# Performance work log

Measured on AMD Instinct MI355X. Metric: run time of the kernel, lower is better.

The kernel has to match this reference:

```python
import jax, jax.numpy as jnp
import numpy as np

N_NODES = 30000


def gcn_conv(x, src, dst, ew, W, b, n):
    # x: [N, Fin] -> linear first (PyG GCNConv), then normalized scatter-add
    h = x @ W  # [N, Fout]
    loops = jnp.arange(n, dtype=src.dtype)
    s = jnp.concatenate([src, loops])
    d = jnp.concatenate([dst, loops])
    w = jnp.concatenate([ew, jnp.ones((n,), dtype=ew.dtype)])
    deg = jax.ops.segment_sum(w, d, num_segments=n)
    dinv = jnp.where(deg > 0, jax.lax.rsqrt(jnp.where(deg > 0, deg, 1.0)), 0.0)
    norm = dinv[s] * w * dinv[d]  # [E+N]
    msg = h[s] * norm[:, None]  # [E+N, Fout]
    out = jax.ops.segment_sum(msg, d, num_segments=n)
    return out + b


def setup_inputs() -> dict:
    key = jax.random.key(0)
    ks = jax.random.split(key, 16)
    n, e, f, c = N_NODES, 480000, 64, 64
    dims = [f, 2 * c, 4 * c, 8 * c]  # 64 -> 128 -> 256 -> 512
    num_classes = 40

    def lin(k, fi, fo):
        k1, k2 = jax.random.split(k)
        s = 1.0 / np.sqrt(fi)
        return (jax.random.uniform(k1, (fi, fo), jnp.float32, -s, s),
                jax.random.uniform(k2, (fo,), jnp.float32, -s, s))

    W1, b1 = lin(ks[0], dims[0], dims[1])
    W2, b2 = lin(ks[1], dims[1], dims[2])
    W3, b3 = lin(ks[2], dims[2], dims[3])
    fW1, fb1 = lin(ks[3], dims[3], dims[3])
    fW2, fb2 = lin(ks[4], dims[3], num_classes)
    return {
        "x": jax.random.normal(ks[5], (n, f), jnp.float32),
        "edge_index": jax.random.randint(ks[6], (2, e), 0, n, jnp.int32),
        "edge_attr": jax.random.uniform(ks[7], (e, 1), jnp.float32),
        "W1": W1, "b1": b1, "W2": W2, "b2": b2, "W3": W3, "b3": b3,
        "fW1": fW1, "fb1": fb1, "fW2": fW2, "fb2": fb2,
    }


def reference(x, edge_index, edge_attr, W1, b1, W2, b2, W3, b3, fW1, fb1, fW2, fb2):
    n = x.shape[0]
    src, dst = edge_index[0], edge_index[1]
    ew = edge_attr.squeeze(-1)
    h = jax.nn.relu(gcn_conv(x, src, dst, ew, W1, b1, n))
    h = jax.nn.relu(gcn_conv(h, src, dst, ew, W2, b2, n))
    h = jax.nn.relu(gcn_conv(h, src, dst, ew, W3, b3, n))
    h = jax.nn.relu(h @ fW1 + fb1)
    h = h @ fW2 + fb2
    return jax.nn.log_softmax(h, axis=1)
```

## Files before the change

### kernel.cpp

```cpp
#include <hip/hip_runtime.h>
#include <cstdint>
#include <cstddef>


typedef _Float16 f16;
typedef _Float16 half8 __attribute__((ext_vector_type(8)));
typedef _Float16 half4 __attribute__((ext_vector_type(4)));
typedef float v4f __attribute__((ext_vector_type(4)));
typedef unsigned long long u64;

__device__ inline void gload_lds16(const void* g, void* l) {
    __builtin_amdgcn_global_load_lds(
        (const __attribute__((address_space(1))) unsigned int*)g,
        (__attribute__((address_space(3))) unsigned int*)l, 16, 0, 0);
}


__global__ __launch_bounds__(256) void k_edge1(const int* __restrict__ dst, const float* __restrict__ ew,
                                               u64* __restrict__ packed4, int* __restrict__ eslot,
                                               int E, int n) {
    int t = blockIdx.x * blockDim.x + threadIdx.x;
    int e0 = t * 4;
    int r = t & 3;
    u64* plane = packed4 + (size_t)r * n;
    if (e0 + 3 < E) {
        int4 d4 = *(const int4*)(dst + e0);
        float4 w4 = *(const float4*)(ew + e0);
        u64 a0 = ((u64)__float2uint_rn(w4.x * 1048576.f) << 24) | 1ULL;
        u64 a1 = ((u64)__float2uint_rn(w4.y * 1048576.f) << 24) | 1ULL;
        u64 a2 = ((u64)__float2uint_rn(w4.z * 1048576.f) << 24) | 1ULL;
        u64 a3 = ((u64)__float2uint_rn(w4.w * 1048576.f) << 24) | 1ULL;
        u64 o0 = atomicAdd(&plane[d4.x], a0);
        u64 o1 = atomicAdd(&plane[d4.y], a1);
        u64 o2 = atomicAdd(&plane[d4.z], a2);
        u64 o3 = atomicAdd(&plane[d4.w], a3);
        int4 s;
        s.x = (int)(o0 & 0xFFFFFF); s.y = (int)(o1 & 0xFFFFFF);
        s.z = (int)(o2 & 0xFFFFFF); s.w = (int)(o3 & 0xFFFFFF);
        *(int4*)(eslot + e0) = s;
    } else {
        for (int e = e0; e < E; ++e) {
            u64 a = ((u64)__float2uint_rn(ew[e] * 1048576.f) << 24) | 1ULL;
            u64 o = atomicAdd(&plane[dst[e]], a);
            eslot[e] = (int)(o & 0xFFFFFF);
        }
    }
}

__global__ __launch_bounds__(256) void k_dinv_scan1(const u64* __restrict__ packed4,
                                                    float* __restrict__ dinv, int* __restrict__ cnt,
                                                    int4* __restrict__ rbase, int* __restrict__ bsum, int n) {
    int i = blockIdx.x * 256 + threadIdx.x;
    int c = 0;
    if (i < n) {
        u64 p0 = packed4[i];
        u64 p1 = packed4[(size_t)n + i];
        u64 p2 = packed4[(size_t)2 * n + i];
        u64 p3 = packed4[(size_t)3 * n + i];
        int c0 = (int)(p0 & 0xFFFFFF), c1 = (int)(p1 & 0xFFFFFF);
        int c2 = (int)(p2 & 0xFFFFFF), c3 = (int)(p3 & 0xFFFFFF);
        c = c0 + c1 + c2 + c3;
        rbase[i] = make_int4(0, c0, c0 + c1, c0 + c1 + c2);
        float d = 1.0f + (float)((p0 >> 24) + (p1 >> 24) + (p2 >> 24) + (p3 >> 24)) * (1.0f / 1048576.f);
        float r = rsqrtf(d);
        r = r * (1.5f - 0.5f * d * r * r);
        dinv[i] = r;
        cnt[i] = c;
    }
    int v = c;
#pragma unroll
    for (int o = 32; o; o >>= 1) v += __shfl_xor(v, o);
    __shared__ int s[4];
    if ((threadIdx.x & 63) == 0) s[threadIdx.x >> 6] = v;
    __syncthreads();
    if (threadIdx.x == 0) bsum[blockIdx.x] = s[0] + s[1] + s[2] + s[3];
}

__device__ inline int block_scan_incl(int v) {
    __shared__ int ws[4];
    int lane = threadIdx.x & 63, w = threadIdx.x >> 6;
#pragma unroll
    for (int off = 1; off < 64; off <<= 1) {
        int t = __shfl_up(v, off);
        if (lane >= off) v += t;
    }
    if (lane == 63) ws[w] = v;
    __syncthreads();
    int add = 0;
#pragma unroll
    for (int i = 0; i < 4; ++i) add += (i < w) ? ws[i] : 0;
    __syncthreads();
    return v + add;
}

__global__ __launch_bounds__(256) void k_scan23(const int* __restrict__ cnt, const int* __restrict__ bsum,
                                                int* __restrict__ rowptr, int n, int E) {
    int blk = blockIdx.x, tid = threadIdx.x;
    int i = blk * 256 + tid;
    __shared__ int spre;
    if (tid < 64) {
        int s = 0;
        for (int j = tid; j < blk; j += 64) s += bsum[j];
#pragma unroll
        for (int o = 32; o; o >>= 1) s += __shfl_xor(s, o);
        if (tid == 0) spre = s;
    }
    __syncthreads();
    int v = (i < n) ? cnt[i] : 0;
    int incl = block_scan_incl(v);
    if (i < n) rowptr[i] = spre + incl - v;
    if (i == n - 1) rowptr[n] = E;
}

__global__ __launch_bounds__(256) void k_fill(const int* __restrict__ src, const int* __restrict__ dst,
                                              const float* __restrict__ ew, const int* __restrict__ eslot,
                                              const float* __restrict__ dinv, const int* __restrict__ rowptr,
                                              const int4* __restrict__ rbase,
                                              int* __restrict__ csr_src, f16* __restrict__ csr_norm, int E) {
    int e = blockIdx.x * blockDim.x + threadIdx.x;
    if (e < E) {
        int d = dst[e], s = src[e];
        int r = (e >> 2) & 3;
        int4 rb = rbase[d];
        int base = (r == 0) ? rb.x : (r == 1) ? rb.y : (r == 2) ? rb.z : rb.w;
        int idx = rowptr[d] + base + eslot[e];
        csr_src[idx] = s;
        csr_norm[idx] = (f16)(dinv[s] * ew[e] * dinv[d]);
    }
}

struct PrepArgs {
    u64* packed4; int n4;
    const float* x; f16* xh; int xt4;
    const float* W[5]; f16* WT[5];
    int lgK[5]; int lgNp[5]; int N[5]; int off[6];
};
__global__ __launch_bounds__(256) void k_prep(PrepArgs a) {
    int i = blockIdx.x * 256 + threadIdx.x;
    if (i < a.n4) { a.packed4[i] = 0ULL; return; }
    int j = i - a.n4;
    if (j < a.xt4) {
        float4 v = *(const float4*)(a.x + (size_t)j * 4);
        half4 h = {(f16)v.x, (f16)v.y, (f16)v.z, (f16)v.w};
        *(half4*)(a.xh + (size_t)j * 4) = h;
        return;
    }
    int w = j - a.xt4;
#pragma unroll
    for (int s = 0; s < 5; ++s) {
        if (w >= a.off[s] && w < a.off[s + 1]) {
            int li = w - a.off[s];
            int Np = 1 << a.lgNp[s];
            int K = 1 << a.lgK[s];
            int k = li >> a.lgNp[s], nr = li & (Np - 1);
            float v = (nr < a.N[s]) ? a.W[s][(size_t)k * a.N[s] + nr] : 0.f;
            a.WT[s][(size_t)nr * K + k] = (f16)v;
        }
    }
}

template <int F>
__global__ __launch_bounds__(256) void k_agg(const f16* __restrict__ h,
                                             const float* __restrict__ dinv, const int* __restrict__ rowptr,
                                             const int* __restrict__ csr_src, const f16* __restrict__ csr_norm,
                                             f16* __restrict__ o, int n) {
    constexpr int LPN = F / 8;
    constexpr int NPW = 64 / LPN;
    int wave = (int)((blockIdx.x * (unsigned)blockDim.x + threadIdx.x) >> 6);
    int lane = threadIdx.x & 63;
    int grp = lane / LPN, lin = lane % LPN;
    int node = wave * NPW + grp;
    if (node >= n) return;
    float di = dinv[node], w0 = di * di;
    float acc[8];
#pragma unroll
    for (int i = 0; i < 8; ++i) acc[i] = 0.f;

    auto gat = [&](int s, float w) {
        half8 x = *(const half8*)(h + (size_t)s * F + lin * 8);
#pragma unroll
        for (int i = 0; i < 8; ++i) acc[i] += w * (float)x[i];
    };

    gat(node, w0);
    int beg = rowptr[node], end = rowptr[node + 1];
    int j = beg;
    for (; j + 3 < end; j += 4) {
        int s0 = csr_src[j], s1 = csr_src[j + 1], s2 = csr_src[j + 2], s3 = csr_src[j + 3];
        float u0 = (float)csr_norm[j], u1 = (float)csr_norm[j + 1];
        float u2 = (float)csr_norm[j + 2], u3 = (float)csr_norm[j + 3];
        gat(s0, u0); gat(s1, u1); gat(s2, u2); gat(s3, u3);
    }
    for (; j < end; ++j) gat(csr_src[j], (float)csr_norm[j]);

    half8 v;
#pragma unroll
    for (int i = 0; i < 8; ++i) v[i] = (f16)acc[i];
    *(half8*)(o + (size_t)node * F + (size_t)lin * 8) = v;
}

template <bool RELU>
__global__ __launch_bounds__(256) void k_mm(const f16* __restrict__ A, const f16* __restrict__ BT,
                                            const float* __restrict__ bias, f16* __restrict__ Ch,
                                            int M, int N, int K, int nB, int nwg) {
    __shared__ f16 lsA[2][128 * 64];
    __shared__ f16 lsB[2][128 * 64];
    int wg = blockIdx.x;
    int q = nwg >> 3, r = nwg & 7;
    int xcd = wg & 7, lin = wg >> 3;
    int wgs = (xcd < r) ? (xcd * (q + 1) + lin) : (r * (q + 1) + (xcd - r) * q + lin);
    int bm = wgs / nB, bn = wgs % nB;

    int tid = threadIdx.x;
    int lane = tid & 63, wid = tid >> 6;
    int l16 = lane & 15, lhi = lane >> 4;
    int wm = (wid >> 1) * 64, wn = (wid & 1) * 64;
    int brow = bm * 128, bcol = bn * 128;

    v4f acc[4][4] = {};

    auto stageA = [&](int buf, int k0) {
#pragma unroll
        for (int it = 0; it < 4; ++it) {
            int b = it * 4096 + tid * 16;
            int row = b >> 7;
            int s = ((b >> 4) & 7) ^ (row & 7);
            gload_lds16(A + (size_t)(brow + row) * K + k0 + s * 8, ((char*)&lsA[buf][0]) + b);
        }
    };
    auto stageB = [&](int buf, int k0) {
#pragma unroll
        for (int it = 0; it < 4; ++it) {
            int b = it * 4096 + tid * 16;
            int row = b >> 7;
            int s = ((b >> 4) & 7) ^ (row & 7);
            gload_lds16(BT + (size_t)(bcol + row) * K + k0 + s * 8, ((char*)&lsB[buf][0]) + b);
        }
    };

    int nk = K >> 6;
    stageA(0, 0);
    stageB(0, 0);
    for (int kt = 0; kt < nk; ++kt) {
        int cur = kt & 1;
        __syncthreads();
        if (kt + 1 < nk) { stageA(cur ^ 1, (kt + 1) << 6); stageB(cur ^ 1, (kt + 1) << 6); }
#pragma unroll
        for (int ks = 0; ks < 2; ++ks) {
            half8 bf[4];
#pragma unroll
            for (int fn = 0; fn < 4; ++fn) {
                int row = wn + fn * 16 + l16;
                int sidx = (ks * 4 + lhi) ^ (row & 7);
                bf[fn] = *(const half8*)(&lsB[cur][0] + row * 64 + sidx * 8);
            }
#pragma unroll
            for (int fm = 0; fm < 4; ++fm) {
                int row = wm + fm * 16 + l16;
                int sidx = (ks * 4 + lhi) ^ (row & 7);
                half8 af = *(const half8*)(&lsA[cur][0] + row * 64 + sidx * 8);
#pragma unroll
                for (int fn = 0; fn < 4; ++fn)
                    acc[fm][fn] = __builtin_amdgcn_mfma_f32_16x16x32_f16(bf[fn], af, acc[fm][fn], 0, 0, 0);
            }
        }
    }
#pragma unroll
    for (int fm = 0; fm < 4; ++fm) {
        int m = brow + wm + fm * 16 + l16;
        if (m >= M) continue;
#pragma unroll
        for (int fn = 0; fn < 4; ++fn) {
            int nb = bcol + wn + fn * 16 + lhi * 4;
            v4f bv = *(const v4f*)(bias + nb);
            v4f v = acc[fm][fn] + bv;
            if (RELU) {
#pragma unroll
                for (int rr = 0; rr < 4; ++rr) v[rr] = fmaxf(v[rr], 0.f);
            }
            half4 hv = {(f16)v[0], (f16)v[1], (f16)v[2], (f16)v[3]};
            *(half4*)(Ch + (size_t)m * N + nb) = hv;
        }
    }
}

__global__ __launch_bounds__(256) void k_mmfc2(const f16* __restrict__ A, const f16* __restrict__ BT,
                                               const float* __restrict__ bias, float* __restrict__ out,
                                               int M, int K) {
    __shared__ f16 lsA[2][256 * 64];
    __shared__ f16 lsB[2][64 * 64];
    int bm = blockIdx.x;
    int tid = threadIdx.x;
    int lane = tid & 63, wid = tid >> 6;
    int l16 = lane & 15, lhi = lane >> 4;
    int wm = wid * 64;
    int brow = bm * 256;

    v4f acc[4][4] = {};

    auto stageA = [&](int buf, int k0) {
#pragma unroll
        for (int it = 0; it < 8; ++it) {
            int b = it * 4096 + tid * 16;
            int row = b >> 7;
            int s = ((b >> 4) & 7) ^ (row & 7);
            gload_lds16(A + (size_t)(brow + row) * K + k0 + s * 8, ((char*)&lsA[buf][0]) + b);
        }
    };
    auto stageB = [&](int buf, int k0) {
#pragma unroll
        for (int it = 0; it < 2; ++it) {
            int b = it * 4096 + tid * 16;
            int row = b >> 7;
            int s = ((b >> 4) & 7) ^ (row & 7);
            gload_lds16(BT + (size_t)row * K + k0 + s * 8, ((char*)&lsB[buf][0]) + b);
        }
    };

    int nk = K >> 6;
    stageA(0, 0);
    stageB(0, 0);
    for (int kt = 0; kt < nk; ++kt) {
        int cur = kt & 1;
        __syncthreads();
        if (kt + 1 < nk) { stageA(cur ^ 1, (kt + 1) << 6); stageB(cur ^ 1, (kt + 1) << 6); }
#pragma unroll
        for (int ks = 0; ks < 2; ++ks) {
            half8 bf[4];
#pragma unroll
            for (int fn = 0; fn < 4; ++fn) {
                int row = fn * 16 + l16;
                int sidx = (ks * 4 + lhi) ^ (row & 7);
                bf[fn] = *(const half8*)(&lsB[cur][0] + row * 64 + sidx * 8);
            }
#pragma unroll
            for (int fm = 0; fm < 4; ++fm) {
                int row = wm + fm * 16 + l16;
                int sidx = (ks * 4 + lhi) ^ (row & 7);
                half8 af = *(const half8*)(&lsA[cur][0] + row * 64 + sidx * 8);
#pragma unroll
                for (int fn = 0; fn < 4; ++fn)
                    acc[fm][fn] = __builtin_amdgcn_mfma_f32_16x16x32_f16(bf[fn], af, acc[fm][fn], 0, 0, 0);
            }
        }
    }

    float bv[4][4];
#pragma unroll
    for (int fn = 0; fn < 4; ++fn)
#pragma unroll
        for (int rr = 0; rr < 4; ++rr) {
            int nn = fn * 16 + lhi * 4 + rr;
            bv[fn][rr] = (nn < 40) ? bias[nn] : 0.f;
        }

#pragma unroll
    for (int fm = 0; fm < 4; ++fm) {
        int m = brow + wm + fm * 16 + l16;
        float v[4][4];
        float mx = -INFINITY;
#pragma unroll
        for (int fn = 0; fn < 4; ++fn)
#pragma unroll
            for (int rr = 0; rr < 4; ++rr) {
                int nn = fn * 16 + lhi * 4 + rr;
                v[fn][rr] = acc[fm][fn][rr] + bv[fn][rr];
                if (nn < 40) mx = fmaxf(mx, v[fn][rr]);
            }
        mx = fmaxf(mx, __shfl_xor(mx, 16));
        mx = fmaxf(mx, __shfl_xor(mx, 32));
        float s = 0.f;
#pragma unroll
        for (int fn = 0; fn < 3; ++fn)
#pragma unroll
            for (int rr = 0; rr < 4; ++rr) {
                int nn = fn * 16 + lhi * 4 + rr;
                if (nn < 40) s += __expf(v[fn][rr] - mx);
            }
        s += __shfl_xor(s, 16);
        s += __shfl_xor(s, 32);
        float ls = __logf(s);
        if (m < M) {
#pragma unroll
            for (int fn = 0; fn < 3; ++fn)
#pragma unroll
                for (int rr = 0; rr < 4; ++rr) {
                    int nn = fn * 16 + lhi * 4 + rr;
                    if (nn < 40) out[(size_t)m * 40 + nn] = v[fn][rr] - mx - ls;
                }
        }
    }
}


extern "C" void kernel_launch(void* const* d_in, const int* in_sizes, int n_in,
                              void* d_out, int out_size, void* d_ws, size_t ws_size,
                              hipStream_t stream) {
    const float* x   = (const float*)d_in[0];
    const int*   ei  = (const int*)d_in[1];
    const float* ea  = (const float*)d_in[2];
    const float* W1  = (const float*)d_in[3];  const float* b1  = (const float*)d_in[4];
    const float* W2  = (const float*)d_in[5];  const float* b2  = (const float*)d_in[6];
    const float* W3  = (const float*)d_in[7];  const float* b3  = (const float*)d_in[8];
    const float* fW1 = (const float*)d_in[9];  const float* fb1 = (const float*)d_in[10];
    const float* fW2 = (const float*)d_in[11]; const float* fb2 = (const float*)d_in[12];

    int n = in_sizes[0] / 64;
    int E = in_sizes[1] / 2;
    int Mpad = ((n + 255) / 256) * 256;
    const int* src = ei;
    const int* dst = ei + E;
    float* out = (float*)d_out;

    char* p = (char*)d_ws;
    auto alloc = [&](size_t bytes) -> char* {
        char* r = p;
        p += (bytes + 255) & ~(size_t)255;
        return r;
    };
    int nb256 = (n + 255) / 256;
    u64*   packed4  = (u64*)alloc((size_t)n * 4 * 8);
    float* dinv     = (float*)alloc((size_t)n * 4);
    int*   cnt      = (int*)alloc((size_t)n * 4);
    int4*  rbase    = (int4*)alloc((size_t)n * 16);
    int*   rowptr   = (int*)alloc((size_t)(n + 1) * 4);
    int*   bsum     = (int*)alloc((size_t)nb256 * 4);
    int*   eslot    = (int*)alloc((size_t)E * 4);
    int*   csr_src  = (int*)alloc((size_t)E * 4);
    f16*   csr_norm = (f16*)alloc((size_t)E * 2);
    f16* XH  = (f16*)alloc((size_t)Mpad * 64 * 2);
    f16* W1T = (f16*)alloc((size_t)128 * 64 * 2);
    f16* W2T = (f16*)alloc((size_t)256 * 128 * 2);
    f16* W3T = (f16*)alloc((size_t)512 * 256 * 2);
    f16* F1T = (f16*)alloc((size_t)512 * 512 * 2);
    f16* F2T = (f16*)alloc((size_t)64 * 512 * 2);
    f16* AGG = (f16*)alloc((size_t)Mpad * 256 * 2);
    f16* HA  = (f16*)alloc((size_t)Mpad * 512 * 2);
    f16* HB  = (f16*)alloc((size_t)Mpad * 512 * 2);

    const int tb = 256;
    int eB = (E + tb - 1) / tb;
    int e4B = (E / 4 + tb - 1) / tb + 1;
    auto aggB = [&](int npw) {
        long waves = (n + npw - 1) / npw;
        return (int)((waves * 64 + tb - 1) / tb);
    };

    {
        PrepArgs a;
        a.packed4 = packed4; a.n4 = n * 4;
        a.x = x; a.xh = XH; a.xt4 = n * 16;
        a.W[0] = W1;  a.WT[0] = W1T; a.lgK[0] = 6; a.lgNp[0] = 7; a.N[0] = 128;
        a.W[1] = W2;  a.WT[1] = W2T; a.lgK[1] = 7; a.lgNp[1] = 8; a.N[1] = 256;
        a.W[2] = W3;  a.WT[2] = W3T; a.lgK[2] = 8; a.lgNp[2] = 9; a.N[2] = 512;
        a.W[3] = fW1; a.WT[3] = F1T; a.lgK[3] = 9; a.lgNp[3] = 9; a.N[3] = 512;
        a.W[4] = fW2; a.WT[4] = F2T; a.lgK[4] = 9; a.lgNp[4] = 6; a.N[4] = 40;
        a.off[0] = 0;
        a.off[1] = a.off[0] + 128 * 64;
        a.off[2] = a.off[1] + 256 * 128;
        a.off[3] = a.off[2] + 512 * 256;
        a.off[4] = a.off[3] + 512 * 512;
        a.off[5] = a.off[4] + 64 * 512;
        int tot = a.n4 + a.xt4 + a.off[5];
        k_prep<<<(tot + tb - 1) / tb, tb, 0, stream>>>(a);
    }

    k_edge1<<<e4B, tb, 0, stream>>>(dst, ea, packed4, eslot, E, n);
    k_dinv_scan1<<<nb256, tb, 0, stream>>>(packed4, dinv, cnt, rbase, bsum, n);
    k_scan23<<<nb256, tb, 0, stream>>>(cnt, bsum, rowptr, n, E);
    k_fill<<<eB, tb, 0, stream>>>(src, dst, ea, eslot, dinv, rowptr, rbase, csr_src, csr_norm, E);

    auto mm = [&](const f16* a, const f16* bt, const float* bias, f16* ch, int N, int K) {
        int nB2 = N / 128;
        int nwg = (Mpad / 128) * nB2;
        k_mm<true><<<nwg, 256, 0, stream>>>(a, bt, bias, ch, n, N, K, nB2, nwg);
    };

    k_agg<64><<<aggB(8), tb, 0, stream>>>(XH, dinv, rowptr, csr_src, csr_norm, AGG, n);
    mm(AGG, W1T, b1, HA, 128, 64);
    k_agg<128><<<aggB(4), tb, 0, stream>>>(HA, dinv, rowptr, csr_src, csr_norm, AGG, n);
    mm(AGG, W2T, b2, HB, 256, 128);
    k_agg<256><<<aggB(2), tb, 0, stream>>>(HB, dinv, rowptr, csr_src, csr_norm, AGG, n);
    mm(AGG, W3T, b3, HA, 512, 256);
    mm(HA, F1T, fb1, HB, 512, 512);
    k_mmfc2<<<Mpad / 256, 256, 0, stream>>>(HB, F2T, fb2, out, n, 512);
}
```

Measured before the change: 199.1 us.

## Use single atomic counter plane and split aggregation accumulators

Replaces the four striped per-node atomic count/degree planes with one plane. This removes the rbase prefix array and its extra loads and stores in the scan and fill kernels, at the cost of more atomic contention per address. The aggregation kernel also unrolls the edge loop by 8 and alternates between two accumulator sets, giving more gathers in flight and shorter FP dependency chains, at the cost of more registers.

New measurement: 204.0 us. +2.5%, slower.

```diff
diff --git a/kernel.cpp b/kernel.cpp
--- a/kernel.cpp
+++ b/kernel.cpp
@@ -17,12 +17,9 @@
 
 
 __global__ __launch_bounds__(256) void k_edge1(const int* __restrict__ dst, const float* __restrict__ ew,
-                                               u64* __restrict__ packed4, int* __restrict__ eslot,
-                                               int E, int n) {
+                                               u64* __restrict__ packed, int* __restrict__ eslot, int E) {
     int t = blockIdx.x * blockDim.x + threadIdx.x;
     int e0 = t * 4;
-    int r = t & 3;
-    u64* plane = packed4 + (size_t)r * n;
     if (e0 + 3 < E) {
         int4 d4 = *(const int4*)(dst + e0);
         float4 w4 = *(const float4*)(ew + e0);
@@ -30,10 +27,10 @@
         u64 a1 = ((u64)__float2uint_rn(w4.y * 1048576.f) << 24) | 1ULL;
         u64 a2 = ((u64)__float2uint_rn(w4.z * 1048576.f) << 24) | 1ULL;
         u64 a3 = ((u64)__float2uint_rn(w4.w * 1048576.f) << 24) | 1ULL;
-        u64 o0 = atomicAdd(&plane[d4.x], a0);
-        u64 o1 = atomicAdd(&plane[d4.y], a1);
-        u64 o2 = atomicAdd(&plane[d4.z], a2);
-        u64 o3 = atomicAdd(&plane[d4.w], a3);
+        u64 o0 = atomicAdd(&packed[d4.x], a0);
+        u64 o1 = atomicAdd(&packed[d4.y], a1);
+        u64 o2 = atomicAdd(&packed[d4.z], a2);
+        u64 o3 = atomicAdd(&packed[d4.w], a3);
         int4 s;
         s.x = (int)(o0 & 0xFFFFFF); s.y = (int)(o1 & 0xFFFFFF);
         s.z = (int)(o2 & 0xFFFFFF); s.w = (int)(o3 & 0xFFFFFF);
@@ -41,27 +38,21 @@
     } else {
         for (int e = e0; e < E; ++e) {
             u64 a = ((u64)__float2uint_rn(ew[e] * 1048576.f) << 24) | 1ULL;
-            u64 o = atomicAdd(&plane[dst[e]], a);
+            u64 o = atomicAdd(&packed[dst[e]], a);
             eslot[e] = (int)(o & 0xFFFFFF);
         }
     }
 }
 
-__global__ __launch_bounds__(256) void k_dinv_scan1(const u64* __restrict__ packed4,
+__global__ __launch_bounds__(256) void k_dinv_scan1(const u64* __restrict__ packed,
                                                     float* __restrict__ dinv, int* __restrict__ cnt,
-                                                    int4* __restrict__ rbase, int* __restrict__ bsum, int n) {
+                                                    int* __restrict__ bsum, int n) {
     int i = blockIdx.x * 256 + threadIdx.x;
     int c = 0;
     if (i < n) {
-        u64 p0 = packed4[i];
-        u64 p1 = packed4[(size_t)n + i];
-        u64 p2 = packed4[(size_t)2 * n + i];
-        u64 p3 = packed4[(size_t)3 * n + i];
-        int c0 = (int)(p0 & 0xFFFFFF), c1 = (int)(p1 & 0xFFFFFF);
-        int c2 = (int)(p2 & 0xFFFFFF), c3 = (int)(p3 & 0xFFFFFF);
-        c = c0 + c1 + c2 + c3;
-        rbase[i] = make_int4(0, c0, c0 + c1, c0 + c1 + c2);
-        float d = 1.0f + (float)((p0 >> 24) + (p1 >> 24) + (p2 >> 24) + (p3 >> 24)) * (1.0f / 1048576.f);
+        u64 pk = packed[i];
+        c = (int)(pk & 0xFFFFFF);
+        float d = 1.0f + (float)(pk >> 24) * (1.0f / 1048576.f);
         float r = rsqrtf(d);
         r = r * (1.5f - 0.5f * d * r * r);
         dinv[i] = r;
@@ -115,30 +106,26 @@
 __global__ __launch_bounds__(256) void k_fill(const int* __restrict__ src, const int* __restrict__ dst,
                                               const float* __restrict__ ew, const int* __restrict__ eslot,
                                               const float* __restrict__ dinv, const int* __restrict__ rowptr,
-                                              const int4* __restrict__ rbase,
                                               int* __restrict__ csr_src, f16* __restrict__ csr_norm, int E) {
     int e = blockIdx.x * blockDim.x + threadIdx.x;
     if (e < E) {
         int d = dst[e], s = src[e];
-        int r = (e >> 2) & 3;
-        int4 rb = rbase[d];
-        int base = (r == 0) ? rb.x : (r == 1) ? rb.y : (r == 2) ? rb.z : rb.w;
-        int idx = rowptr[d] + base + eslot[e];
+        int idx = rowptr[d] + eslot[e];
         csr_src[idx] = s;
         csr_norm[idx] = (f16)(dinv[s] * ew[e] * dinv[d]);
     }
 }
 
 struct PrepArgs {
-    u64* packed4; int n4;
+    u64* packed; int n;
     const float* x; f16* xh; int xt4;
     const float* W[5]; f16* WT[5];
     int lgK[5]; int lgNp[5]; int N[5]; int off[6];
 };
 __global__ __launch_bounds__(256) void k_prep(PrepArgs a) {
     int i = blockIdx.x * 256 + threadIdx.x;
-    if (i < a.n4) { a.packed4[i] = 0ULL; return; }
-    int j = i - a.n4;
+    if (i < a.n) { a.packed[i] = 0ULL; return; }
+    int j = i - a.n;
     if (j < a.xt4) {
         float4 v = *(const float4*)(a.x + (size_t)j * 4);
         half4 h = {(f16)v.x, (f16)v.y, (f16)v.z, (f16)v.w};
@@ -172,30 +159,39 @@
     int node = wave * NPW + grp;
     if (node >= n) return;
     float di = dinv[node], w0 = di * di;
-    float acc[8];
-#pragma unroll
-    for (int i = 0; i < 8; ++i) acc[i] = 0.f;
-
-    auto gat = [&](int s, float w) {
+    float acca[8], accb[8];
+#pragma unroll
+    for (int i = 0; i < 8; ++i) { acca[i] = 0.f; accb[i] = 0.f; }
+
+    auto gat = [&](float* acc, int s, float w) {
         half8 x = *(const half8*)(h + (size_t)s * F + lin * 8);
 #pragma unroll
         for (int i = 0; i < 8; ++i) acc[i] += w * (float)x[i];
     };
 
-    gat(node, w0);
+    gat(acca, node, w0);
     int beg = rowptr[node], end = rowptr[node + 1];
     int j = beg;
-    for (; j + 3 < end; j += 4) {
+    for (; j + 7 < end; j += 8) {
         int s0 = csr_src[j], s1 = csr_src[j + 1], s2 = csr_src[j + 2], s3 = csr_src[j + 3];
+        int s4 = csr_src[j + 4], s5 = csr_src[j + 5], s6 = csr_src[j + 6], s7 = csr_src[j + 7];
         float u0 = (float)csr_norm[j], u1 = (float)csr_norm[j + 1];
         float u2 = (float)csr_norm[j + 2], u3 = (float)csr_norm[j + 3];
-        gat(s0, u0); gat(s1, u1); gat(s2, u2); gat(s3, u3);
-    }
-    for (; j < end; ++j) gat(csr_src[j], (float)csr_norm[j]);
+        float u4 = (float)csr_norm[j + 4], u5 = (float)csr_norm[j + 5];
+        float u6 = (float)csr_norm[j + 6], u7 = (float)csr_norm[j + 7];
+        gat(acca, s0, u0); gat(accb, s1, u1); gat(acca, s2, u2); gat(accb, s3, u3);
+        gat(acca, s4, u4); gat(accb, s5, u5); gat(acca, s6, u6); gat(accb, s7, u7);
+    }
+    for (; j + 1 < end; j += 2) {
+        int s0 = csr_src[j], s1 = csr_src[j + 1];
+        float u0 = (float)csr_norm[j], u1 = (float)csr_norm[j + 1];
+        gat(acca, s0, u0); gat(accb, s1, u1);
+    }
+    if (j < end) gat(acca, csr_src[j], (float)csr_norm[j]);
 
     half8 v;
 #pragma unroll
-    for (int i = 0; i < 8; ++i) v[i] = (f16)acc[i];
+    for (int i = 0; i < 8; ++i) v[i] = (f16)(acca[i] + accb[i]);
     *(half8*)(o + (size_t)node * F + (size_t)lin * 8) = v;
 }
 
@@ -419,10 +415,9 @@
         return r;
     };
     int nb256 = (n + 255) / 256;
-    u64*   packed4  = (u64*)alloc((size_t)n * 4 * 8);
+    u64*   packed   = (u64*)alloc((size_t)n * 8);
     float* dinv     = (float*)alloc((size_t)n * 4);
     int*   cnt      = (int*)alloc((size_t)n * 4);
-    int4*  rbase    = (int4*)alloc((size_t)n * 16);
     int*   rowptr   = (int*)alloc((size_t)(n + 1) * 4);
     int*   bsum     = (int*)alloc((size_t)nb256 * 4);
     int*   eslot    = (int*)alloc((size_t)E * 4);
@@ -448,7 +443,7 @@
 
     {
         PrepArgs a;
-        a.packed4 = packed4; a.n4 = n * 4;
+        a.packed = packed; a.n = n;
         a.x = x; a.xh = XH; a.xt4 = n * 16;
         a.W[0] = W1;  a.WT[0] = W1T; a.lgK[0] = 6; a.lgNp[0] = 7; a.N[0] = 128;
         a.W[1] = W2;  a.WT[1] = W2T; a.lgK[1] = 7; a.lgNp[1] = 8; a.N[1] = 256;
@@ -461,14 +456,14 @@
         a.off[3] = a.off[2] + 512 * 256;
         a.off[4] = a.off[3] + 512 * 512;
         a.off[5] = a.off[4] + 64 * 512;
-        int tot = a.n4 + a.xt4 + a.off[5];
+        int tot = a.n + a.xt4 + a.off[5];
         k_prep<<<(tot + tb - 1) / tb, tb, 0, stream>>>(a);
     }
 
-    k_edge1<<<e4B, tb, 0, stream>>>(dst, ea, packed4, eslot, E, n);
-    k_dinv_scan1<<<nb256, tb, 0, stream>>>(packed4, dinv, cnt, rbase, bsum, n);
+    k_edge1<<<e4B, tb, 0, stream>>>(dst, ea, packed, eslot, E);
+    k_dinv_scan1<<<nb256, tb, 0, stream>>>(packed, dinv, cnt, bsum, n);
     k_scan23<<<nb256, tb, 0, stream>>>(cnt, bsum, rowptr, n, E);
-    k_fill<<<eB, tb, 0, stream>>>(src, dst, ea, eslot, dinv, rowptr, rbase, csr_src, csr_norm, E);
+    k_fill<<<eB, tb, 0, stream>>>(src, dst, ea, eslot, dinv, rowptr, csr_src, csr_norm, E);
 
     auto mm = [&](const f16* a, const f16* bt, const float* bias, f16* ch, int N, int K) {
         int nB2 = N / 128;
```
